# Kernel optimization log

Measured on AMD Instinct MI355X. Metric: run time of the kernel, lower is better.

## Reference

```python
import jax, jax.numpy as jnp
import numpy as np

H = 16  # num_heads


def setup_inputs() -> dict:
    key = jax.random.key(0)
    ks = jax.random.split(key, 8)
    B, S, d, L = 1, 2048, 1024, 8
    hd = d // H
    s = 0.02
    return {
        "x": jax.random.normal(ks[0], (B, S, d), jnp.float32),
        "past_values": jax.random.normal(ks[1], (L, B, H, S, hd), jnp.float32),
        "Wqkv": jax.random.normal(ks[2], (3 * d, d), jnp.float32) * s,
        "bqkv": jax.random.normal(ks[3], (3 * d,), jnp.float32) * s,
        "Wcol": jax.random.normal(ks[4], (d, d), jnp.float32) * s,
        "bcol": jax.random.normal(ks[5], (d,), jnp.float32) * s,
        "Wout": jax.random.normal(ks[6], (d, d), jnp.float32) * s,
        "bout": jax.random.normal(ks[7], (d,), jnp.float32) * s,
    }


def reference(x, past_values, Wqkv, bqkv, Wcol, bcol, Wout, bout):
    B, S, d = x.shape
    L = past_values.shape[0]
    hd = d // H
    scale = 1.0 / np.sqrt(hd).astype(np.float32)

    qkv = x @ Wqkv.T + bqkv                       # [B,S,3d]
    q, k, v = jnp.split(qkv, 3, axis=-1)

    def heads(t):                                  # [B,S,d] -> [B,H,S,hd]
        return t.reshape(B, S, H, hd).transpose(0, 2, 1, 3)

    q_row, k, v = heads(q), heads(k), heads(v)
    q_col = heads(x @ Wcol.T + bcol)

    # causal token scores [B,H,S,S]
    token_scores = jnp.einsum('bhqd,bhkd->bhqk', q_row, k) * scale
    causal = jnp.triu(jnp.ones((S, S), bool), 1)
    token_scores = jnp.where(causal, -jnp.inf, token_scores)

    # stack past values: torch stack(dim=3) -> [B,H,S,L,hd]; permute -> [B,S,L,H*hd]
    pv = past_values.transpose(1, 3, 0, 2, 4).reshape(B, S, L, d)
    ri = pv.reshape(B, S * L, d)
    mu = ri.mean(-1, keepdims=True)
    var = ri.var(-1, keepdims=True)
    ri = (ri - mu) / jnp.sqrt(var + 1e-5)          # F.layer_norm, no affine

    Wk, bk = Wqkv[d:2 * d], bqkv[d:2 * d]
    Wv, bv = Wqkv[2 * d:], bqkv[2 * d:]
    rk = (ri @ Wk.T + bk).reshape(B, S * L, H, hd).transpose(0, 2, 1, 3).reshape(B, H, S, L, hd)
    rv = (ri @ Wv.T + bv).reshape(B, S * L, H, hd).transpose(0, 2, 1, 3).reshape(B, H, S, L, hd)

    mem_scores = jnp.einsum('bhsd,bhsld->bhsl', q_col, rk) * scale  # [B,H,S,L]

    scores = jnp.concatenate([token_scores, mem_scores], axis=-1)   # [B,H,S,S+L]
    w = jax.nn.softmax(scores, axis=-1)
    tw, mw = w[..., :S], w[..., S:]

    ctx = jnp.einsum('bhqk,bhkd->bhqd', tw, v) + jnp.einsum('bhsl,bhsld->bhsd', mw, rv)
    out = ctx.transpose(0, 2, 1, 3).reshape(B, S, d)
    return out @ Wout.T + bout
```

## Files before the change

kernel.cpp:

```cpp
#include <hip/hip_runtime.h>
#include <math.h>

#define D   1024
#define H   16
#define HD  64
#define SEQ 2048
#define LL  8
#define SCALE 0.125f

typedef __attribute__((ext_vector_type(8))) __bf16 bf16x8;
typedef __attribute__((ext_vector_type(4))) float floatx4;
typedef __attribute__((ext_vector_type(8))) unsigned short ushort8;

__device__ inline unsigned short f32_to_bf16(float f) {
    unsigned int u = __builtin_bit_cast(unsigned int, f);
    u += 0x7FFF + ((u >> 16) & 1);
    return (unsigned short)(u >> 16);
}
__device__ inline float bf2f(unsigned short u) {
    unsigned int x = (unsigned int)u << 16;
    return __builtin_bit_cast(float, x);
}
__device__ inline void load_lds16(const void* g, void* l) {
    __builtin_amdgcn_global_load_lds(
        (__attribute__((address_space(1))) void*)g,
        (__attribute__((address_space(3))) void*)l, 16, 0, 0);
}

__device__ inline void xcd_swizzle(int& bx, int& by) {
    const int gx   = gridDim.x;
    const int lin  = blockIdx.y * gx + blockIdx.x;
    const int nblk = gx * gridDim.y;
    const int virt = (lin & 7) * (nblk >> 3) + (lin >> 3);
    bx = virt % gx;
    by = virt / gx;
}

#define NQ_X    524288
#define NQ_WQKV 786432
#define NQ_WC   262144
#define NQ_WO   262144
#define LN_BLK  16384
#define CVT_BLK 7168
#define PREP_GRID (LN_BLK + CVT_BLK + 4)

__global__ __launch_bounds__(256) void prep_kernel(
    const float* __restrict__ pv, const float* __restrict__ x,
    const float* __restrict__ Wqkv, const float* __restrict__ Wcol,
    const float* __restrict__ Wout, const float* __restrict__ bqkv,
    const float* __restrict__ bcol,
    unsigned short* __restrict__ ri, unsigned short* __restrict__ xb,
    unsigned short* __restrict__ W4b, unsigned short* __restrict__ Woutb,
    float* __restrict__ b4)
{
    const int b = blockIdx.x;
    const int t = threadIdx.x;
    if (b < LN_BLK) {
        const int r = b;
        const int s = r >> 3, l = r & 7;
        const int h = t >> 4, e = (t & 15) * 4;
        const size_t src = (size_t)l * (H * SEQ * HD) + (size_t)h * (SEQ * HD)
                         + (size_t)s * HD + e;
        float4 v = *(const float4*)(pv + src);
        float sum = v.x + v.y + v.z + v.w;
        float sq  = v.x * v.x + v.y * v.y + v.z * v.z + v.w * v.w;
#pragma unroll
        for (int off = 32; off; off >>= 1) {
            sum += __shfl_xor(sum, off);
            sq  += __shfl_xor(sq, off);
        }
        __shared__ float red[8];
        if ((t & 63) == 0) { red[(t >> 6) * 2] = sum; red[(t >> 6) * 2 + 1] = sq; }
        __syncthreads();
        sum = red[0] + red[2] + red[4] + red[6];
        sq  = red[1] + red[3] + red[5] + red[7];
        const float mean = sum * (1.f / 1024.f);
        const float var  = sq * (1.f / 1024.f) - mean * mean;
        const float rstd = rsqrtf(var + 1e-5f);
        ushort4 o;
        o.x = f32_to_bf16((v.x - mean) * rstd);
        o.y = f32_to_bf16((v.y - mean) * rstd);
        o.z = f32_to_bf16((v.z - mean) * rstd);
        o.w = f32_to_bf16((v.w - mean) * rstd);
        *(ushort4*)(ri + (size_t)r * D + t * 4) = o;
    } else if (b < LN_BLK + CVT_BLK) {
        const int i = (b - LN_BLK) * 256 + t;
        const float* src; unsigned short* dst; int off;
        if (i < NQ_X)                        { src = x;    dst = xb;    off = i; }
        else if (i < NQ_X + NQ_WQKV)         { src = Wqkv; dst = W4b;   off = i - NQ_X; }
        else if (i < NQ_X + NQ_WQKV + NQ_WC) { src = Wcol; dst = W4b;   off = i - NQ_X;
                                               src = Wcol; off = i - NQ_X - NQ_WQKV;
                                               dst = W4b + (size_t)NQ_WQKV * 4 / 1;
                                               {
                                                   float4 v = ((const float4*)Wcol)[i - NQ_X - NQ_WQKV];
                                                   ushort4 o;
                                                   o.x = f32_to_bf16(v.x); o.y = f32_to_bf16(v.y);
                                                   o.z = f32_to_bf16(v.z); o.w = f32_to_bf16(v.w);
                                                   ((ushort4*)(W4b))[NQ_WQKV + (i - NQ_X - NQ_WQKV)] = o;
                                               }
                                               return; }
        else                                 { src = Wout; dst = Woutb; off = i - NQ_X - NQ_WQKV - NQ_WC; }
        float4 v = ((const float4*)src)[off];
        ushort4 o;
        o.x = f32_to_bf16(v.x); o.y = f32_to_bf16(v.y);
        o.z = f32_to_bf16(v.z); o.w = f32_to_bf16(v.w);
        ((ushort4*)dst)[off] = o;
    } else {
        const int q = (b - LN_BLK - CVT_BLK) * 256 + t;
        float4 v = (q < 768) ? ((const float4*)bqkv)[q] : ((const float4*)bcol)[q - 768];
        ((float4*)b4)[q] = v;
    }
}

template <typename CT>
__global__ __launch_bounds__(256) void gemm_bf16_kernel(
    const unsigned short* __restrict__ A, const unsigned short* __restrict__ W,
    const float* __restrict__ bias, CT* __restrict__ C, int K, int N)
{
    __shared__ unsigned short As[128 * 32];
    __shared__ unsigned short Ws[128 * 32];
    const int t    = threadIdx.x;
    const int wave = t >> 6, lane = t & 63;
    const int wm   = wave >> 1, wn = wave & 1;
    int bx, by;
    xcd_swizzle(bx, by);
    const int m0 = by * 128, n0 = bx * 128;

    floatx4 acc[4][4];
#pragma unroll
    for (int i = 0; i < 4; i++)
#pragma unroll
        for (int j = 0; j < 4; j++) acc[i][j] = (floatx4)0.f;

    const int lrow = lane >> 2;
    const int lcol = (lane & 3) * 8;
    const unsigned short* Ag = A + (size_t)(m0 + wave * 32 + lrow) * K + lcol;
    const unsigned short* Wg = W + (size_t)(n0 + wave * 32 + lrow) * K + lcol;
    unsigned short* Asw = &As[wave * 32 * 32];
    unsigned short* Wsw = &Ws[wave * 32 * 32];
    const size_t rowskip = (size_t)16 * K;

    const int arow  = lane & 15;
    const int aquad = (lane >> 4) * 8;

    for (int k0 = 0; k0 < K; k0 += 32) {
        load_lds16(Ag + k0,           Asw);
        load_lds16(Ag + k0 + rowskip, Asw + 16 * 32);
        load_lds16(Wg + k0,           Wsw);
        load_lds16(Wg + k0 + rowskip, Wsw + 16 * 32);
        __syncthreads();

        bf16x8 af[4], wf[4];
#pragma unroll
        for (int mi = 0; mi < 4; mi++)
            af[mi] = *(const bf16x8*)&As[(wm * 64 + mi * 16 + arow) * 32 + aquad];
#pragma unroll
        for (int ni = 0; ni < 4; ni++)
            wf[ni] = *(const bf16x8*)&Ws[(wn * 64 + ni * 16 + arow) * 32 + aquad];
#pragma unroll
        for (int mi = 0; mi < 4; mi++)
#pragma unroll
            for (int ni = 0; ni < 4; ni++)
                acc[mi][ni] = __builtin_amdgcn_mfma_f32_16x16x32_bf16(
                    af[mi], wf[ni], acc[mi][ni], 0, 0, 0);
        __syncthreads();
    }

    const int crow = (lane >> 4) * 4, ccol = lane & 15;
#pragma unroll
    for (int mi = 0; mi < 4; mi++) {
#pragma unroll
        for (int ni = 0; ni < 4; ni++) {
            const int gm = m0 + wm * 64 + mi * 16 + crow;
            const int gn = n0 + wn * 64 + ni * 16 + ccol;
            const float bb = bias[gn];
#pragma unroll
            for (int r = 0; r < 4; r++) {
                float v = acc[mi][ni][r] + bb;
                if constexpr (sizeof(CT) == 2)
                    C[(size_t)(gm + r) * N + gn] = (CT)f32_to_bf16(v);
                else
                    C[(size_t)(gm + r) * N + gn] = v;
            }
        }
    }
}

union AttnShared {
    struct { unsigned short Qs[64 * 72]; unsigned short Ks[64 * 72]; } qk;
    float Osp[64 * 68];
};

__global__ __launch_bounds__(256) void attn_split_kernel(
    const unsigned short* __restrict__ qkv4, const unsigned short* __restrict__ rkv,
    float* __restrict__ Opart, float2* __restrict__ mlpart)
{
    const int t    = threadIdx.x;
    const int w    = t >> 6, lane = t & 63;
    const int lrow = lane & 15;
    const int lk   = (lane >> 4) * 8;
    const int rrow = (lane >> 4) * 4;
    const int lin  = blockIdx.x;
    const int hs   = lin & 31, g = lin >> 5;
    const int h    = hs >> 1, s = hs & 1;
    const int a    = g & 7, bq = g >> 3;
    const int qt   = (bq == 0) ? a : (bq == 1) ? 15 - a : (bq == 2) ? 16 + a : 31 - a;
    const int q0   = qt * 64;
    const int n    = qt + 1, nh = (n + 1) >> 1;
    const int lo   = s ? nh : 0, hi = s ? n : nh;
    const int part = (h * 32 + qt) * 2 + s;

    __shared__ AttnShared U;
    __shared__ unsigned short Vt[64 * 72];
    __shared__ unsigned short Pb[64 * 72];
    __shared__ float row_m[64], row_l[64];
    __shared__ float mem_mm[64], mem_alpha[64], mem_suml[64], mem_p[64 * 8];

#pragma unroll
    for (int p = 0; p < 2; p++) {
        int idx = p * 256 + t;
        int row = idx >> 3, col = (idx & 7) * 8;
        *(bf16x8*)&U.qk.Qs[row * 72 + col] =
            *(const bf16x8*)(qkv4 + (size_t)(q0 + row) * 4096 + h * HD + col);
    }

    float m_i[4], l_i[4];
    floatx4 Oacc[4];
#pragma unroll
    for (int r = 0; r < 4; r++) { m_i[r] = -1e30f; l_i[r] = 0.f; }
#pragma unroll
    for (int et = 0; et < 4; et++) Oacc[et] = (floatx4)0.f;

    for (int jt = lo; jt < hi; jt++) {
        const int j0 = jt * 64;
#pragma unroll
        for (int p = 0; p < 2; p++) {
            int idx = p * 256 + t;
            int row = idx >> 3, col = (idx & 7) * 8;
            *(bf16x8*)&U.qk.Ks[row * 72 + col] =
                *(const bf16x8*)(qkv4 + (size_t)(j0 + row) * 4096 + D + h * HD + col);
        }
        {
            const int pr = t & 31, eg = t >> 5;
            const unsigned short* v0 =
                qkv4 + (size_t)(j0 + 2 * pr) * 4096 + 2 * D + h * HD + eg * 8;
            ushort8 va = *(const ushort8*)v0;
            ushort8 vb = *(const ushort8*)(v0 + 4096);
#pragma unroll
            for (int j = 0; j < 8; j++) {
                unsigned int pk = (unsigned int)va[j] | ((unsigned int)vb[j] << 16);
                *(unsigned int*)&Vt[(eg * 8 + j) * 72 + 2 * pr] = pk;
            }
        }
        __syncthreads();

        floatx4 S[4];
#pragma unroll
        for (int nt = 0; nt < 4; nt++) S[nt] = (floatx4)0.f;
#pragma unroll
        for (int kst = 0; kst < 2; kst++) {
            bf16x8 aq = *(const bf16x8*)&U.qk.Qs[(w * 16 + lrow) * 72 + kst * 32 + lk];
#pragma unroll
            for (int nt = 0; nt < 4; nt++) {
                bf16x8 bk = *(const bf16x8*)&U.qk.Ks[(nt * 16 + lrow) * 72 + kst * 32 + lk];
                S[nt] = __builtin_amdgcn_mfma_f32_16x16x32_bf16(aq, bk, S[nt], 0, 0, 0);
            }
        }

#pragma unroll
        for (int r = 0; r < 4; r++) {
            const int qg = q0 + w * 16 + rrow + r;
            float sc[4];
            float mx = -1e30f;
#pragma unroll
            for (int nt = 0; nt < 4; nt++) {
                sc[nt] = S[nt][r] * SCALE;
                if (j0 + nt * 16 + lrow > qg) sc[nt] = -1e30f;
                mx = fmaxf(mx, sc[nt]);
            }
#pragma unroll
            for (int off = 1; off < 16; off <<= 1)
                mx = fmaxf(mx, __shfl_xor(mx, off));
            if (mx <= -1e29f) {
#pragma unroll
                for (int nt = 0; nt < 4; nt++)
                    Pb[(w * 16 + rrow + r) * 72 + nt * 16 + lrow] = 0;
                continue;
            }
            const float newm  = fmaxf(m_i[r], mx);
            const float alpha = __expf(m_i[r] - newm);
            m_i[r] = newm;
            float ps = 0.f;
#pragma unroll
            for (int nt = 0; nt < 4; nt++) {
                float pe = __expf(sc[nt] - newm);
                ps += pe;
                Pb[(w * 16 + rrow + r) * 72 + nt * 16 + lrow] = f32_to_bf16(pe);
            }
#pragma unroll
            for (int off = 1; off < 16; off <<= 1)
                ps += __shfl_xor(ps, off);
            l_i[r] = l_i[r] * alpha + ps;
#pragma unroll
            for (int et = 0; et < 4; et++) Oacc[et][r] *= alpha;
        }
        __syncthreads();

#pragma unroll
        for (int kst = 0; kst < 2; kst++) {
            bf16x8 ap = *(const bf16x8*)&Pb[(w * 16 + lrow) * 72 + kst * 32 + lk];
#pragma unroll
            for (int et = 0; et < 4; et++) {
                bf16x8 bv = *(const bf16x8*)&Vt[(et * 16 + lrow) * 72 + kst * 32 + lk];
                Oacc[et] = __builtin_amdgcn_mfma_f32_16x16x32_bf16(ap, bv, Oacc[et], 0, 0, 0);
            }
        }
        __syncthreads();
    }

    if (s == 1) {
#pragma unroll
        for (int r = 0; r < 4; r++) {
            const int ql = w * 16 + rrow + r;
            if (lrow == 0) mlpart[(size_t)part * 64 + ql] = make_float2(m_i[r], l_i[r]);
#pragma unroll
            for (int et = 0; et < 4; et++)
                Opart[((size_t)part * 64 + ql) * 64 + et * 16 + lrow] = Oacc[et][r];
        }
        return;
    }

#pragma unroll
    for (int r = 0; r < 4; r++) {
        const int ql = w * 16 + rrow + r;
        if (lrow == 0) { row_m[ql] = m_i[r]; row_l[ql] = l_i[r]; }
#pragma unroll
        for (int et = 0; et < 4; et++)
            U.Osp[ql * 68 + et * 16 + lrow] = Oacc[et][r];
    }
    __syncthreads();

    {
        const int qi = t >> 2, quad = t & 3;
        const int qg = q0 + qi;
        float qv[16];
        const unsigned short* qcp = qkv4 + (size_t)qg * 4096 + 3 * D + h * HD + quad * 16;
        ushort8 qa = *(const ushort8*)qcp;
        ushort8 qb = *(const ushort8*)(qcp + 8);
#pragma unroll
        for (int j = 0; j < 8; j++) {
            qv[j]     = bf2f(qa[j]) * SCALE;
            qv[8 + j] = bf2f(qb[j]) * SCALE;
        }
        float ms[8];
#pragma unroll
        for (int l = 0; l < 8; l++) {
            const unsigned short* rr = rkv + (size_t)(qg * LL + l) * 2048 + h * HD + quad * 16;
            ushort8 ra = *(const ushort8*)rr;
            ushort8 rb = *(const ushort8*)(rr + 8);
            float pacc = 0.f;
#pragma unroll
            for (int j = 0; j < 8; j++)
                pacc += qv[j] * bf2f(ra[j]) + qv[8 + j] * bf2f(rb[j]);
            pacc += __shfl_xor(pacc, 1);
            pacc += __shfl_xor(pacc, 2);
            ms[l] = pacc;
        }
        const float mo = row_m[qi];
        float mm = mo;
#pragma unroll
        for (int l = 0; l < 8; l++) mm = fmaxf(mm, ms[l]);
        const float alpha = __expf(mo - mm);
        float suml = 0.f;
        float pl[8];
#pragma unroll
        for (int l = 0; l < 8; l++) { pl[l] = __expf(ms[l] - mm); suml += pl[l]; }
        if (quad == 0) {
            mem_mm[qi]    = mm;
            mem_alpha[qi] = alpha;
            mem_suml[qi]  = suml;
#pragma unroll
            for (int l = 0; l < 8; l++) mem_p[qi * 8 + l] = pl[l];
        }
    }
    __syncthreads();

    {
        const int tx = t & 15, ty = t >> 4;
#pragma unroll
        for (int i = 0; i < 4; i++) {
            const int qi = ty * 4 + i, qg = q0 + qi;
            const float alpha = mem_alpha[qi];
            const float lf = row_l[qi] * alpha + mem_suml[qi];
            float4 o = *(const float4*)&U.Osp[qi * 68 + tx * 4];
            o.x *= alpha; o.y *= alpha; o.z *= alpha; o.w *= alpha;
#pragma unroll
            for (int l = 0; l < 8; l++) {
                const float p = mem_p[qi * 8 + l];
                ushort4 vb = *(const ushort4*)(rkv + (size_t)(qg * LL + l) * 2048
                                               + D + h * HD + tx * 4);
                o.x = fmaf(p, bf2f(vb.x), o.x);
                o.y = fmaf(p, bf2f(vb.y), o.y);
                o.z = fmaf(p, bf2f(vb.z), o.z);
                o.w = fmaf(p, bf2f(vb.w), o.w);
            }
            *(float4*)&Opart[((size_t)part * 64 + qi) * 64 + tx * 4] = o;
            if (tx == 0) mlpart[(size_t)part * 64 + qi] = make_float2(mem_mm[qi], lf);
        }
    }
}

__global__ __launch_bounds__(256) void attn_merge_kernel(
    const float* __restrict__ Opart, const float2* __restrict__ mlpart,
    unsigned short* __restrict__ ctx)
{
    const int blk = blockIdx.x;
    const int h = blk >> 5, qt = blk & 31;
    const int q0 = qt * 64;
    const int t = threadIdx.x, tx = t & 15, ty = t >> 4;
    const size_t p0 = (size_t)blk * 2, p1 = p0 + 1;
#pragma unroll
    for (int i = 0; i < 4; i++) {
        const int qi = ty * 4 + i, qg = q0 + qi;
        float2 ml0 = mlpart[p0 * 64 + qi];
        float2 ml1 = mlpart[p1 * 64 + qi];
        const float M  = fmaxf(ml0.x, ml1.x);
        const float f0 = __expf(ml0.x - M), f1 = __expf(ml1.x - M);
        const float rl = 1.f / (ml0.y * f0 + ml1.y * f1);
        float4 o0 = *(const float4*)&Opart[(p0 * 64 + qi) * 64 + tx * 4];
        float4 o1 = *(const float4*)&Opart[(p1 * 64 + qi) * 64 + tx * 4];
        ushort4 ob;
        ob.x = f32_to_bf16((o0.x * f0 + o1.x * f1) * rl);
        ob.y = f32_to_bf16((o0.y * f0 + o1.y * f1) * rl);
        ob.z = f32_to_bf16((o0.z * f0 + o1.z * f1) * rl);
        ob.w = f32_to_bf16((o0.w * f0 + o1.w * f1) * rl);
        *(ushort4*)(ctx + (size_t)qg * D + h * HD + tx * 4) = ob;
    }
}

extern "C" void kernel_launch(void* const* d_in, const int* in_sizes, int n_in,
                              void* d_out, int out_size, void* d_ws, size_t ws_size,
                              hipStream_t stream)
{
    const float* x    = (const float*)d_in[0];
    const float* pv   = (const float*)d_in[1];
    const float* Wqkv = (const float*)d_in[2];
    const float* bqkv = (const float*)d_in[3];
    const float* Wcol = (const float*)d_in[4];
    const float* bcol = (const float*)d_in[5];
    const float* Wout = (const float*)d_in[6];
    const float* bout = (const float*)d_in[7];
    float* out = (float*)d_out;

    char* p = (char*)d_ws;
    unsigned short* x_bf    = (unsigned short*)p; p += (size_t)2048 * 1024 * 2;
    unsigned short* W4_bf   = (unsigned short*)p; p += (size_t)4096 * 1024 * 2;
    unsigned short* Wout_bf = (unsigned short*)p; p += (size_t)1024 * 1024 * 2;
    float*          b4      = (float*)p;          p += (size_t)4096 * 4;
    unsigned short* ri_bf   = (unsigned short*)p; p += (size_t)16384 * 1024 * 2;
    unsigned short* qkv4_bf = (unsigned short*)p; p += (size_t)2048 * 4096 * 2;
    unsigned short* rkv_bf  = (unsigned short*)p; p += (size_t)16384 * 2048 * 2;
    unsigned short* ctx_bf  = (unsigned short*)p; p += (size_t)2048 * 1024 * 2;
    float*          Opart   = (float*)p;          p += (size_t)1024 * 64 * 64 * 4;
    float2*         mlpart  = (float2*)p;         p += (size_t)1024 * 64 * 8;

    prep_kernel<<<PREP_GRID, 256, 0, stream>>>(pv, x, Wqkv, Wcol, Wout, bqkv, bcol,
                                               ri_bf, x_bf, W4_bf, Wout_bf, b4);
    gemm_bf16_kernel<unsigned short><<<dim3(32, 16), 256, 0, stream>>>(
        x_bf, W4_bf, b4, qkv4_bf, 1024, 4096);
    gemm_bf16_kernel<unsigned short><<<dim3(16, 128), 256, 0, stream>>>(
        ri_bf, W4_bf + (size_t)1024 * 1024, bqkv + 1024, rkv_bf, 1024, 2048);
    attn_split_kernel<<<1024, 256, 0, stream>>>(qkv4_bf, rkv_bf, Opart, mlpart);
    attn_merge_kernel<<<512, 256, 0, stream>>>(Opart, mlpart, ctx_bf);
    gemm_bf16_kernel<float><<<dim3(8, 16), 256, 0, stream>>>(
        ctx_bf, Wout_bf, bout, out, 1024, 1024);
}
```

Before: 363.8 us.

## Reassociate memory-key/value projections to avoid materializing rk/rv for all memory rows

Instead of running a large GEMM that projects all S*L normalized memory rows through Wk and Wv, the memory scores are computed as (q_col·Wk_h) dotted with ri, using a per-head transformed query U built by a batched GEMM against a transposed Wk. The memory context is computed by first forming weighted sums of ri per head (rbar) and then applying Wv in a smaller GEMM, with the bias scaled by the total memory probability. This removes the 16384x1024x2048 GEMM and its output buffer. In exchange it adds several kernels, a 64 MB U/rbar intermediate buffer, an fp32 token-context round trip, and extra launches.

```diff
diff --git a/kernel.cpp b/kernel.cpp
--- a/kernel.cpp
+++ b/kernel.cpp
@@ -88,17 +88,14 @@
         const float* src; unsigned short* dst; int off;
         if (i < NQ_X)                        { src = x;    dst = xb;    off = i; }
         else if (i < NQ_X + NQ_WQKV)         { src = Wqkv; dst = W4b;   off = i - NQ_X; }
-        else if (i < NQ_X + NQ_WQKV + NQ_WC) { src = Wcol; dst = W4b;   off = i - NQ_X;
-                                               src = Wcol; off = i - NQ_X - NQ_WQKV;
-                                               dst = W4b + (size_t)NQ_WQKV * 4 / 1;
-                                               {
-                                                   float4 v = ((const float4*)Wcol)[i - NQ_X - NQ_WQKV];
-                                                   ushort4 o;
-                                                   o.x = f32_to_bf16(v.x); o.y = f32_to_bf16(v.y);
-                                                   o.z = f32_to_bf16(v.z); o.w = f32_to_bf16(v.w);
-                                                   ((ushort4*)(W4b))[NQ_WQKV + (i - NQ_X - NQ_WQKV)] = o;
-                                               }
-                                               return; }
+        else if (i < NQ_X + NQ_WQKV + NQ_WC) {
+            float4 v = ((const float4*)Wcol)[i - NQ_X - NQ_WQKV];
+            ushort4 o;
+            o.x = f32_to_bf16(v.x); o.y = f32_to_bf16(v.y);
+            o.z = f32_to_bf16(v.z); o.w = f32_to_bf16(v.w);
+            ((ushort4*)(W4b))[NQ_WQKV + (i - NQ_X - NQ_WQKV)] = o;
+            return;
+        }
         else                                 { src = Wout; dst = Woutb; off = i - NQ_X - NQ_WQKV - NQ_WC; }
         float4 v = ((const float4*)src)[off];
         ushort4 o;
@@ -112,11 +109,49 @@
     }
 }
 
-template <typename CT>
+__global__ __launch_bounds__(256) void wkt_kernel(
+    const float* __restrict__ Wqkv, unsigned short* __restrict__ WkT)
+{
+    const int h = blockIdx.x >> 4, ct = blockIdx.x & 15;
+    const int c0 = ct * 64;
+    const int t = threadIdx.x;
+    __shared__ float tile[64][68];
+    {
+        const int e  = t >> 2;
+        const int c4 = (t & 3) * 16;
+        const float* src = Wqkv + (size_t)(D + h * HD + e) * D + c0 + c4;
+#pragma unroll
+        for (int j = 0; j < 4; j++) {
+            float4 v = ((const float4*)src)[j];
+            *(float4*)&tile[e][c4 + j * 4] = v;
+        }
+    }
+    __syncthreads();
+    {
+        const int c  = t >> 2;
+        const int e0 = (t & 3) * 16;
+        ushort8 o0, o1;
+#pragma unroll
+        for (int j = 0; j < 8; j++) o0[j] = f32_to_bf16(tile[e0 + j][c]);
+#pragma unroll
+        for (int j = 0; j < 8; j++) o1[j] = f32_to_bf16(tile[e0 + 8 + j][c]);
+        unsigned short* dst = WkT + (size_t)h * (D * HD) + (size_t)(c0 + c) * HD + e0;
+        *(ushort8*)dst       = o0;
+        *(ushort8*)(dst + 8) = o1;
+    }
+}
+
+template <typename CT, bool HAS_BIAS>
 __global__ __launch_bounds__(256) void gemm_bf16_kernel(
     const unsigned short* __restrict__ A, const unsigned short* __restrict__ W,
-    const float* __restrict__ bias, CT* __restrict__ C, int K, int N)
-{
+    const float* __restrict__ bias, CT* __restrict__ C,
+    int K, int N, int lda, int ldw, int ldc,
+    size_t zsA, size_t zsW, size_t zsC)
+{
+    A += (size_t)blockIdx.z * zsA;
+    W += (size_t)blockIdx.z * zsW;
+    C += (size_t)blockIdx.z * zsC;
+
     __shared__ unsigned short As[128 * 32];
     __shared__ unsigned short Ws[128 * 32];
     const int t    = threadIdx.x;
@@ -134,20 +169,21 @@
 
     const int lrow = lane >> 2;
     const int lcol = (lane & 3) * 8;
-    const unsigned short* Ag = A + (size_t)(m0 + wave * 32 + lrow) * K + lcol;
-    const unsigned short* Wg = W + (size_t)(n0 + wave * 32 + lrow) * K + lcol;
+    const unsigned short* Ag = A + (size_t)(m0 + wave * 32 + lrow) * lda + lcol;
+    const unsigned short* Wg = W + (size_t)(n0 + wave * 32 + lrow) * ldw + lcol;
     unsigned short* Asw = &As[wave * 32 * 32];
     unsigned short* Wsw = &Ws[wave * 32 * 32];
-    const size_t rowskip = (size_t)16 * K;
+    const size_t rowskipA = (size_t)16 * lda;
+    const size_t rowskipW = (size_t)16 * ldw;
 
     const int arow  = lane & 15;
     const int aquad = (lane >> 4) * 8;
 
     for (int k0 = 0; k0 < K; k0 += 32) {
-        load_lds16(Ag + k0,           Asw);
-        load_lds16(Ag + k0 + rowskip, Asw + 16 * 32);
-        load_lds16(Wg + k0,           Wsw);
-        load_lds16(Wg + k0 + rowskip, Wsw + 16 * 32);
+        load_lds16(Ag + k0,             Asw);
+        load_lds16(Ag + k0 + rowskipA,  Asw + 16 * 32);
+        load_lds16(Wg + k0,             Wsw);
+        load_lds16(Wg + k0 + rowskipW,  Wsw + 16 * 32);
         __syncthreads();
 
         bf16x8 af[4], wf[4];
@@ -173,17 +209,68 @@
         for (int ni = 0; ni < 4; ni++) {
             const int gm = m0 + wm * 64 + mi * 16 + crow;
             const int gn = n0 + wn * 64 + ni * 16 + ccol;
-            const float bb = bias[gn];
+            float bb = 0.f;
+            if constexpr (HAS_BIAS) bb = bias[gn];
 #pragma unroll
             for (int r = 0; r < 4; r++) {
                 float v = acc[mi][ni][r] + bb;
                 if constexpr (sizeof(CT) == 2)
-                    C[(size_t)(gm + r) * N + gn] = (CT)f32_to_bf16(v);
+                    C[(size_t)(gm + r) * ldc + gn] = (CT)f32_to_bf16(v);
                 else
-                    C[(size_t)(gm + r) * N + gn] = v;
-            }
-        }
-    }
+                    C[(size_t)(gm + r) * ldc + gn] = v;
+            }
+        }
+    }
+}
+
+#define RI_STRIDE 1032
+
+__global__ __launch_bounds__(256) void memsc_kernel(
+    const unsigned short* __restrict__ U, const unsigned short* __restrict__ ri,
+    const unsigned short* __restrict__ qkv4, const float* __restrict__ bqkv,
+    float* __restrict__ scores)
+{
+    const int s = blockIdx.x;
+    const int t = threadIdx.x;
+    __shared__ unsigned short riS[LL * RI_STRIDE];
+    __shared__ float qbS[H];
+    {
+        const unsigned short* src = ri + (size_t)s * (LL * D);
+#pragma unroll
+        for (int j = 0; j < 4; j++) {
+            const int off = (j * 256 + t) * 8;
+            const int l = off >> 10, c = off & 1023;
+            ushort8 v = *(const ushort8*)(src + off);
+            *(ushort8*)&riS[l * RI_STRIDE + c] = v;
+        }
+    }
+    {
+        const int h = t >> 4, sub = t & 15;
+        const unsigned short* qc = qkv4 + (size_t)s * 4096 + 3 * D + h * HD + sub * 4;
+        const float* bk = bqkv + D + h * HD + sub * 4;
+        float acc = 0.f;
+#pragma unroll
+        for (int j = 0; j < 4; j++) acc += bf2f(qc[j]) * bk[j];
+#pragma unroll
+        for (int off = 1; off < 16; off <<= 1) acc += __shfl_xor(acc, off);
+        if (sub == 0) qbS[h] = acc;
+    }
+    __syncthreads();
+    const int p = t >> 1, half = t & 1;
+    const int h = p >> 3, l = p & 7;
+    const unsigned short* Up = U + ((size_t)h * SEQ + s) * D + half * 512;
+    const unsigned short* rp = &riS[l * RI_STRIDE + half * 512];
+    float acc = 0.f;
+#pragma unroll 4
+    for (int j = 0; j < 64; j++) {
+        ushort8 u = *(const ushort8*)(Up + j * 8);
+        ushort8 r = *(const ushort8*)(rp + j * 8);
+#pragma unroll
+        for (int k = 0; k < 8; k++) acc += bf2f(u[k]) * bf2f(r[k]);
+    }
+    acc += __shfl_xor(acc, 1);
+    if (half == 0)
+        scores[((size_t)s * H + h) * LL + l] = (acc + qbS[h]) * SCALE;
 }
 
 union AttnShared {
@@ -192,7 +279,8 @@
 };
 
 __global__ __launch_bounds__(256) void attn_split_kernel(
-    const unsigned short* __restrict__ qkv4, const unsigned short* __restrict__ rkv,
+    const unsigned short* __restrict__ qkv4,
+    const float* __restrict__ mem_scores, float* __restrict__ memP,
     float* __restrict__ Opart, float2* __restrict__ mlpart)
 {
     const int t    = threadIdx.x;
@@ -214,7 +302,7 @@
     __shared__ unsigned short Vt[64 * 72];
     __shared__ unsigned short Pb[64 * 72];
     __shared__ float row_m[64], row_l[64];
-    __shared__ float mem_mm[64], mem_alpha[64], mem_suml[64], mem_p[64 * 8];
+    __shared__ float mem_mm[64], mem_alpha[64], mem_suml[64];
 
 #pragma unroll
     for (int p = 0; p < 2; p++) {
@@ -340,48 +428,26 @@
     }
     __syncthreads();
 
-    {
-        const int qi = t >> 2, quad = t & 3;
-        const int qg = q0 + qi;
-        float qv[16];
-        const unsigned short* qcp = qkv4 + (size_t)qg * 4096 + 3 * D + h * HD + quad * 16;
-        ushort8 qa = *(const ushort8*)qcp;
-        ushort8 qb = *(const ushort8*)(qcp + 8);
-#pragma unroll
-        for (int j = 0; j < 8; j++) {
-            qv[j]     = bf2f(qa[j]) * SCALE;
-            qv[8 + j] = bf2f(qb[j]) * SCALE;
-        }
-        float ms[8];
-#pragma unroll
-        for (int l = 0; l < 8; l++) {
-            const unsigned short* rr = rkv + (size_t)(qg * LL + l) * 2048 + h * HD + quad * 16;
-            ushort8 ra = *(const ushort8*)rr;
-            ushort8 rb = *(const ushort8*)(rr + 8);
-            float pacc = 0.f;
-#pragma unroll
-            for (int j = 0; j < 8; j++)
-                pacc += qv[j] * bf2f(ra[j]) + qv[8 + j] * bf2f(rb[j]);
-            pacc += __shfl_xor(pacc, 1);
-            pacc += __shfl_xor(pacc, 2);
-            ms[l] = pacc;
-        }
+    if (t < 64) {
+        const int qi = t, qg = q0 + qi;
+        const float* msp = mem_scores + ((size_t)qg * H + h) * LL;
+        float ms[LL];
+#pragma unroll
+        for (int l = 0; l < LL; l++) ms[l] = msp[l];
         const float mo = row_m[qi];
         float mm = mo;
 #pragma unroll
-        for (int l = 0; l < 8; l++) mm = fmaxf(mm, ms[l]);
+        for (int l = 0; l < LL; l++) mm = fmaxf(mm, ms[l]);
         const float alpha = __expf(mo - mm);
         float suml = 0.f;
-        float pl[8];
-#pragma unroll
-        for (int l = 0; l < 8; l++) { pl[l] = __expf(ms[l] - mm); suml += pl[l]; }
-        if (quad == 0) {
-            mem_mm[qi]    = mm;
-            mem_alpha[qi] = alpha;
-            mem_suml[qi]  = suml;
-#pragma unroll
-            for (int l = 0; l < 8; l++) mem_p[qi * 8 + l] = pl[l];
-        }
+        float* mp = memP + ((size_t)qg * H + h) * LL;
+#pragma unroll
+        for (int l = 0; l < LL; l++) {
+            float pe = __expf(ms[l] - mm);
+            suml += pe;
+            mp[l] = pe;
+        }
+        mem_mm[qi] = mm; mem_alpha[qi] = alpha; mem_suml[qi] = suml;
     }
     __syncthreads();
 
@@ -389,21 +455,11 @@
         const int tx = t & 15, ty = t >> 4;
 #pragma unroll
         for (int i = 0; i < 4; i++) {
-            const int qi = ty * 4 + i, qg = q0 + qi;
+            const int qi = ty * 4 + i;
             const float alpha = mem_alpha[qi];
             const float lf = row_l[qi] * alpha + mem_suml[qi];
             float4 o = *(const float4*)&U.Osp[qi * 68 + tx * 4];
             o.x *= alpha; o.y *= alpha; o.z *= alpha; o.w *= alpha;
-#pragma unroll
-            for (int l = 0; l < 8; l++) {
-                const float p = mem_p[qi * 8 + l];
-                ushort4 vb = *(const ushort4*)(rkv + (size_t)(qg * LL + l) * 2048
-                                               + D + h * HD + tx * 4);
-                o.x = fmaf(p, bf2f(vb.x), o.x);
-                o.y = fmaf(p, bf2f(vb.y), o.y);
-                o.z = fmaf(p, bf2f(vb.z), o.z);
-                o.w = fmaf(p, bf2f(vb.w), o.w);
-            }
             *(float4*)&Opart[((size_t)part * 64 + qi) * 64 + tx * 4] = o;
             if (tx == 0) mlpart[(size_t)part * 64 + qi] = make_float2(mem_mm[qi], lf);
         }
@@ -412,7 +468,8 @@
 
 __global__ __launch_bounds__(256) void attn_merge_kernel(
     const float* __restrict__ Opart, const float2* __restrict__ mlpart,
-    unsigned short* __restrict__ ctx)
+    const float* __restrict__ memP,
+    float* __restrict__ tok, float* __restrict__ mwf, float* __restrict__ Pmem)
 {
     const int blk = blockIdx.x;
     const int h = blk >> 5, qt = blk & 31;
@@ -429,12 +486,132 @@
         const float rl = 1.f / (ml0.y * f0 + ml1.y * f1);
         float4 o0 = *(const float4*)&Opart[(p0 * 64 + qi) * 64 + tx * 4];
         float4 o1 = *(const float4*)&Opart[(p1 * 64 + qi) * 64 + tx * 4];
-        ushort4 ob;
-        ob.x = f32_to_bf16((o0.x * f0 + o1.x * f1) * rl);
-        ob.y = f32_to_bf16((o0.y * f0 + o1.y * f1) * rl);
-        ob.z = f32_to_bf16((o0.z * f0 + o1.z * f1) * rl);
-        ob.w = f32_to_bf16((o0.w * f0 + o1.w * f1) * rl);
-        *(ushort4*)(ctx + (size_t)qg * D + h * HD + tx * 4) = ob;
+        float4 o;
+        o.x = (o0.x * f0 + o1.x * f1) * rl;
+        o.y = (o0.y * f0 + o1.y * f1) * rl;
+        o.z = (o0.z * f0 + o1.z * f1) * rl;
+        o.w = (o0.w * f0 + o1.w * f1) * rl;
+        *(float4*)&tok[(size_t)qg * D + h * HD + tx * 4] = o;
+        if (tx == 0) {
+            const float w0 = f0 * rl;
+            const float* mp = memP + ((size_t)qg * H + h) * LL;
+            float* mw = mwf + ((size_t)qg * H + h) * LL;
+            float psum = 0.f;
+#pragma unroll
+            for (int l = 0; l < LL; l++) { float v = mp[l] * w0; mw[l] = v; psum += v; }
+            Pmem[(size_t)qg * H + h] = psum;
+        }
+    }
+}
+
+__global__ __launch_bounds__(256) void rbar_kernel(
+    const float* __restrict__ mwf, const unsigned short* __restrict__ ri,
+    unsigned short* __restrict__ rbar)
+{
+    const int s = blockIdx.x, t = threadIdx.x;
+    __shared__ unsigned short riS[LL * D];
+    __shared__ float wS[H * LL];
+    {
+        const unsigned short* src = ri + (size_t)s * (LL * D);
+#pragma unroll
+        for (int j = 0; j < 4; j++) {
+            const int off = (j * 256 + t) * 8;
+            *(ushort8*)&riS[off] = *(const ushort8*)(src + off);
+        }
+    }
+    if (t < H * LL) wS[t] = mwf[(size_t)s * (H * LL) + t];
+    __syncthreads();
+    const int c4 = t * 4;
+#pragma unroll
+    for (int hh = 0; hh < H; hh++) {
+        float v0 = 0.f, v1 = 0.f, v2 = 0.f, v3 = 0.f;
+#pragma unroll
+        for (int l = 0; l < LL; l++) {
+            const float wv = wS[hh * LL + l];
+            ushort4 rr = *(const ushort4*)&riS[l * D + c4];
+            v0 += wv * bf2f(rr.x); v1 += wv * bf2f(rr.y);
+            v2 += wv * bf2f(rr.z); v3 += wv * bf2f(rr.w);
+        }
+        ushort4 o;
+        o.x = f32_to_bf16(v0); o.y = f32_to_bf16(v1);
+        o.z = f32_to_bf16(v2); o.w = f32_to_bf16(v3);
+        *(ushort4*)(rbar + ((size_t)hh * SEQ + s) * D + c4) = o;
+    }
+}
+
+__global__ __launch_bounds__(256) void gemm_ctx_kernel(
+    const unsigned short* __restrict__ rbar, const unsigned short* __restrict__ W4,
+    const float* __restrict__ bqkv, const float* __restrict__ Pmem,
+    const float* __restrict__ tok, unsigned short* __restrict__ ctx)
+{
+    const int mt = blockIdx.x;
+    const int h  = blockIdx.y;
+    const unsigned short* A  = rbar + (size_t)h * SEQ * D + (size_t)mt * 128 * D;
+    const unsigned short* Wv = W4 + (size_t)(2 * D + h * HD) * D;
+    const float* bv = bqkv + 2 * D + h * HD;
+
+    __shared__ unsigned short As[128 * 32];
+    __shared__ unsigned short Ws[64 * 32];
+    const int t    = threadIdx.x;
+    const int wave = t >> 6, lane = t & 63;
+
+    floatx4 acc[2][4];
+#pragma unroll
+    for (int i = 0; i < 2; i++)
+#pragma unroll
+        for (int j = 0; j < 4; j++) acc[i][j] = (floatx4)0.f;
+
+    const int lrow = lane >> 2;
+    const int lcol = (lane & 3) * 8;
+    const unsigned short* Ag = A  + (size_t)(wave * 32 + lrow) * D + lcol;
+    const unsigned short* Wg = Wv + (size_t)(wave * 32 + lrow) * D + lcol;
+    unsigned short* Asw = &As[wave * 32 * 32];
+    unsigned short* Wsw = &Ws[wave * 32 * 32];
+    const size_t rowskip = (size_t)16 * D;
+
+    const int arow  = lane & 15;
+    const int aquad = (lane >> 4) * 8;
+
+    for (int k0 = 0; k0 < D; k0 += 32) {
+        load_lds16(Ag + k0,           Asw);
+        load_lds16(Ag + k0 + rowskip, Asw + 16 * 32);
+        if (wave < 2) {
+            load_lds16(Wg + k0,           Wsw);
+            load_lds16(Wg + k0 + rowskip, Wsw + 16 * 32);
+        }
+        __syncthreads();
+
+        bf16x8 af[2], wf[4];
+#pragma unroll
+        for (int mi = 0; mi < 2; mi++)
+            af[mi] = *(const bf16x8*)&As[(wave * 32 + mi * 16 + arow) * 32 + aquad];
+#pragma unroll
+        for (int ni = 0; ni < 4; ni++)
+            wf[ni] = *(const bf16x8*)&Ws[(ni * 16 + arow) * 32 + aquad];
+#pragma unroll
+        for (int mi = 0; mi < 2; mi++)
+#pragma unroll
+            for (int ni = 0; ni < 4; ni++)
+                acc[mi][ni] = __builtin_amdgcn_mfma_f32_16x16x32_bf16(
+                    af[mi], wf[ni], acc[mi][ni], 0, 0, 0);
+        __syncthreads();
+    }
+
+    const int crow = (lane >> 4) * 4, ccol = lane & 15;
+#pragma unroll
+    for (int mi = 0; mi < 2; mi++) {
+#pragma unroll
+        for (int ni = 0; ni < 4; ni++) {
+            const int e  = ni * 16 + ccol;
+            const float bb = bv[e];
+#pragma unroll
+            for (int r = 0; r < 4; r++) {
+                const int grow = mt * 128 + wave * 32 + mi * 16 + crow + r;
+                float v = acc[mi][ni][r] + bb * Pmem[(size_t)grow * H + h]
+                          + tok[(size_t)grow * D + h * HD + e];
+                ctx[(size_t)grow * D + h * HD + e] = f32_to_bf16(v);
+            }
+        }
     }
 }
 
@@ -459,19 +636,30 @@
     float*          b4      = (float*)p;          p += (size_t)4096 * 4;
     unsigned short* ri_bf   = (unsigned short*)p; p += (size_t)16384 * 1024 * 2;
     unsigned short* qkv4_bf = (unsigned short*)p; p += (size_t)2048 * 4096 * 2;
-    unsigned short* rkv_bf  = (unsigned short*)p; p += (size_t)16384 * 2048 * 2;
+    unsigned short* WkT_bf  = (unsigned short*)p; p += (size_t)16 * 1024 * 64 * 2;
+    float*          scores  = (float*)p;          p += (size_t)2048 * 16 * 8 * 4;
+    float*          memP    = (float*)p;          p += (size_t)2048 * 16 * 8 * 4;
+    float*          mwf     = (float*)p;          p += (size_t)2048 * 16 * 8 * 4;
+    float*          Pmem    = (float*)p;          p += (size_t)2048 * 16 * 4;
+    float*          tok     = (float*)p;          p += (size_t)2048 * 1024 * 4;
     unsigned short* ctx_bf  = (unsigned short*)p; p += (size_t)2048 * 1024 * 2;
     float*          Opart   = (float*)p;          p += (size_t)1024 * 64 * 64 * 4;
     float2*         mlpart  = (float2*)p;         p += (size_t)1024 * 64 * 8;
+    unsigned short* Urb     = (unsigned short*)p; p += (size_t)16 * 2048 * 1024 * 2;
 
     prep_kernel<<<PREP_GRID, 256, 0, stream>>>(pv, x, Wqkv, Wcol, Wout, bqkv, bcol,
                                                ri_bf, x_bf, W4_bf, Wout_bf, b4);
-    gemm_bf16_kernel<unsigned short><<<dim3(32, 16), 256, 0, stream>>>(
-        x_bf, W4_bf, b4, qkv4_bf, 1024, 4096);
-    gemm_bf16_kernel<unsigned short><<<dim3(16, 128), 256, 0, stream>>>(
-        ri_bf, W4_bf + (size_t)1024 * 1024, bqkv + 1024, rkv_bf, 1024, 2048);
-    attn_split_kernel<<<1024, 256, 0, stream>>>(qkv4_bf, rkv_bf, Opart, mlpart);
-    attn_merge_kernel<<<512, 256, 0, stream>>>(Opart, mlpart, ctx_bf);
-    gemm_bf16_kernel<float><<<dim3(8, 16), 256, 0, stream>>>(
-        ctx_bf, Wout_bf, bout, out, 1024, 1024);
-}
+    wkt_kernel<<<256, 256, 0, stream>>>(Wqkv, WkT_bf);
+    gemm_bf16_kernel<unsigned short, true><<<dim3(32, 16, 1), 256, 0, stream>>>(
+        x_bf, W4_bf, b4, qkv4_bf, 1024, 4096, 1024, 1024, 4096, 0, 0, 0);
+    gemm_bf16_kernel<unsigned short, false><<<dim3(8, 16, 16), 256, 0, stream>>>(
+        qkv4_bf + 3 * D, WkT_bf, nullptr, Urb, 64, 1024, 4096, 64, 1024,
+        (size_t)HD, (size_t)D * HD, (size_t)SEQ * D);
+    memsc_kernel<<<2048, 256, 0, stream>>>(Urb, ri_bf, qkv4_bf, bqkv, scores);
+    attn_split_kernel<<<1024, 256, 0, stream>>>(qkv4_bf, scores, memP, Opart, mlpart);
+    attn_merge_kernel<<<512, 256, 0, stream>>>(Opart, mlpart, memP, tok, mwf, Pmem);
+    rbar_kernel<<<2048, 256, 0, stream>>>(mwf, ri_bf, Urb);
+    gemm_ctx_kernel<<<dim3(16, 16), 256, 0, stream>>>(Urb, W4_bf, bqkv, Pmem, tok, ctx_bf);
+    gemm_bf16_kernel<float, true><<<dim3(8, 16, 1), 256, 0, stream>>>(
+        ctx_bf, Wout_bf, bout, out, 1024, 1024, 1024, 1024, 1024, 0, 0, 0);
+}
```

After: 365.5 us. About the same (+0.5%).
